# Performance work log

Hardware: AMD Instinct MI355X
Metric: run time of the kernel (lower is better)

The kernel has to match this reference:

```python
import jax, jax.numpy as jnp
import numpy as np

NH = 4        # router attention heads
M1, M2 = 16, 16  # Fourier modes kept
N_FNO_LAYERS = 4
TOP_K = 2
TEMP = 1.0


def _ln(x, g, b):
    m = x.mean(-1, keepdims=True)
    v = ((x - m) ** 2).mean(-1, keepdims=True)
    return (x - m) / jnp.sqrt(v + 1e-5) * g + b


def _mha(s, wqkv, bqkv, wo, bo):
    B, S, D = s.shape
    dh = D // NH
    qkv = s @ wqkv + bqkv
    q, k, v = jnp.split(qkv, 3, axis=-1)
    rs = lambda t: t.reshape(B, S, NH, dh).transpose(0, 2, 1, 3)
    q, k, v = rs(q), rs(k), rs(v)
    a = jax.nn.softmax(jnp.einsum('bhqd,bhkd->bhqk', q, k) / np.sqrt(dh), axis=-1)
    o = jnp.einsum('bhqk,bhkd->bhqd', a, v).transpose(0, 2, 1, 3).reshape(B, S, D)
    return o @ wo + bo


def _spectral_conv(h, w1, w2):
    # h: (B, Ci, H, W); w1/w2: (Ci, Co, M1, M2, 2) real/imag pairs
    B, Ci, H, W = h.shape
    Co = w1.shape[1]
    ft = jnp.fft.rfft2(h, axes=(-2, -1))  # (B, Ci, H, W//2+1) complex
    w1c = w1[..., 0] + 1j * w1[..., 1]
    w2c = w2[..., 0] + 1j * w2[..., 1]
    lo = jnp.einsum('bixy,ioxy->boxy', ft[:, :, :M1, :M2], w1c)
    hi = jnp.einsum('bixy,ioxy->boxy', ft[:, :, -M1:, :M2], w2c)
    oft = jnp.zeros((B, Co, H, W // 2 + 1), dtype=ft.dtype)
    oft = oft.at[:, :, :M1, :M2].set(lo).at[:, :, -M1:, :M2].set(hi)
    return jnp.fft.irfft2(oft, s=(H, W), axes=(-2, -1))


def _fno(x, lw, lb, sw1, sw2, kw, kb, p1w, p1b, p2w, p2b):
    h = jnp.einsum('bchw,co->bohw', x, lw) + lb[None, :, None, None]
    for l in range(N_FNO_LAYERS):
        s = _spectral_conv(h, sw1[l], sw2[l])
        sk = jnp.einsum('bchw,co->bohw', h, kw[l]) + kb[l][None, :, None, None]
        h = s + sk
        if l < N_FNO_LAYERS - 1:
            h = jax.nn.gelu(h)
    h = jax.nn.gelu(jnp.einsum('bchw,co->bohw', h, p1w) + p1b[None, :, None, None])
    return jnp.einsum('bchw,co->bohw', h, p2w) + p2b[None, :, None, None]


def _router(x, enc_in_w, enc_in_b, attn_wqkv, attn_bqkv, attn_wo, attn_bo,
            ln1_g, ln1_b, ffn_w1, ffn_b1, ffn_w2, ffn_b2, ln2_g, ln2_b, fc_w, fc_b):
    ic = x[:, :, 0, :]                       # (B, C, W) initial condition
    s = ic.transpose(0, 2, 1) @ enc_in_w + enc_in_b  # (B, W, hd)
    for l in range(attn_wqkv.shape[0]):
        s = _ln(s + _mha(s, attn_wqkv[l], attn_bqkv[l], attn_wo[l], attn_bo[l]), ln1_g[l], ln1_b[l])
        f = jax.nn.relu(s @ ffn_w1[l] + ffn_b1[l]) @ ffn_w2[l] + ffn_b2[l]
        s = _ln(s + f, ln2_g[l], ln2_b[l])
    feat = s.max(axis=1)                     # global max-pool over sequence
    logits = feat @ fc_w + fc_b              # (B, E)
    vals, idx = jax.lax.top_k(logits, TOP_K)
    w = jax.nn.softmax(vals / TEMP, axis=-1)
    B = logits.shape[0]
    rw = jnp.zeros_like(logits).at[jnp.arange(B)[:, None], idx].set(w)
    return rw


def setup_inputs() -> dict:
    key = jax.random.key(0)
    ks = iter(jax.random.split(key, 40))
    B, C, H, W = 32, 1, 64, 64
    E, HC, HD, RL, FF, OC = 8, 64, 64, 2, 256, 1
    rn = lambda shp, sc: jax.random.normal(next(ks), shp, dtype=jnp.float32) * sc
    inp = {
        'x': rn((B, C, H, W), 1.0),
        'enc_in_w': rn((C, HD), 0.5), 'enc_in_b': jnp.zeros((HD,), jnp.float32),
        'attn_wqkv': rn((RL, HD, 3 * HD), 0.08), 'attn_bqkv': jnp.zeros((RL, 3 * HD), jnp.float32),
        'attn_wo': rn((RL, HD, HD), 0.08), 'attn_bo': jnp.zeros((RL, HD), jnp.float32),
        'ln1_g': jnp.ones((RL, HD), jnp.float32), 'ln1_b': jnp.zeros((RL, HD), jnp.float32),
        'ffn_w1': rn((RL, HD, FF), 0.08), 'ffn_b1': jnp.zeros((RL, FF), jnp.float32),
        'ffn_w2': rn((RL, FF, HD), 0.05), 'ffn_b2': jnp.zeros((RL, HD), jnp.float32),
        'ln2_g': jnp.ones((RL, HD), jnp.float32), 'ln2_b': jnp.zeros((RL, HD), jnp.float32),
        'fc_w': rn((HD, E), 0.1), 'fc_b': jnp.zeros((E,), jnp.float32),
        'lift_w': rn((E, C, HC), 0.3), 'lift_b': jnp.zeros((E, HC), jnp.float32),
        'spec_w1': rn((E, N_FNO_LAYERS, HC, HC, M1, M2, 2), 1.0 / HC),
        'spec_w2': rn((E, N_FNO_LAYERS, HC, HC, M1, M2, 2), 1.0 / HC),
        'skip_w': rn((E, N_FNO_LAYERS, HC, HC), 0.08), 'skip_b': jnp.zeros((E, N_FNO_LAYERS, HC), jnp.float32),
        'proj1_w': rn((E, HC, HC), 0.08), 'proj1_b': jnp.zeros((E, HC), jnp.float32),
        'proj2_w': rn((E, HC, OC), 0.08), 'proj2_b': jnp.zeros((E, OC), jnp.float32),
    }
    return inp


def reference(x, enc_in_w, enc_in_b, attn_wqkv, attn_bqkv, attn_wo, attn_bo,
              ln1_g, ln1_b, ffn_w1, ffn_b1, ffn_w2, ffn_b2, ln2_g, ln2_b, fc_w, fc_b,
              lift_w, lift_b, spec_w1, spec_w2, skip_w, skip_b,
              proj1_w, proj1_b, proj2_w, proj2_b):
    rw = _router(x, enc_in_w, enc_in_b, attn_wqkv, attn_bqkv, attn_wo, attn_bo,
                 ln1_g, ln1_b, ffn_w1, ffn_b1, ffn_w2, ffn_b2, ln2_g, ln2_b, fc_w, fc_b)
    E = rw.shape[1]
    out = jnp.zeros((x.shape[0], proj2_w.shape[2], x.shape[2], x.shape[3]), x.dtype)
    for e in range(E):
        # weight is 0 for non-selected experts, so dense weighted sum == masked dispatch
        y = _fno(x, lift_w[e], lift_b[e], spec_w1[e], spec_w2[e],
                 skip_w[e], skip_b[e], proj1_w[e], proj1_b[e], proj2_w[e], proj2_b[e])
        out = out + rw[:, e, None, None, None] * y
    return out
```

## Files before the change

kernel.cpp:

```cpp
#include <hip/hip_runtime.h>
#include <math.h>

#define TWOPI_F 6.283185307179586f
#define LD4(p) (*(const float4*)(p))

__device__ __forceinline__ float gelu_f(float v) {
    float u = 0.7978845608028654f * (v + 0.044715f * v * v * v);
    return 0.5f * v * (1.f + tanhf(u));
}

__global__ void init_tables_kernel(float* __restrict__ Wy, float* __restrict__ TWX,
                                   float* __restrict__ WY2) {
    int t = threadIdx.x;
    for (int i = t; i < 1024; i += 256) {
        int y = i >> 4, k = i & 15;
        int m = (k * y) & 63;
        float a = -TWOPI_F * (float)m / 64.f;
        Wy[y * 32 + 2 * k]     = cosf(a);
        Wy[y * 32 + 2 * k + 1] = sinf(a);
    }
    if (t < 64) {
        float a = -TWOPI_F * (float)t / 64.f;
        TWX[2 * t]           = cosf(a);
        TWX[2 * t + 1]       = sinf(a);
        TWX[128 + 2 * t]     = cosf(a);
        TWX[128 + 2 * t + 1] = -sinf(a);
    }
    for (int i = t; i < 1024; i += 256) {
        int y = i >> 4, k = i & 15;
        int m = (k * y) & 63;
        float a = TWOPI_F * (float)m / 64.f;
        float sc = (k == 0 ? 1.f : 2.f) / 4096.f;
        WY2[y * 32 + 2 * k]     = sc * cosf(a);
        WY2[y * 32 + 2 * k + 1] = sc * sinf(a);
    }
}

__global__ __launch_bounds__(512) void router_kernel(
    const float* __restrict__ x, const float* __restrict__ enc_w, const float* __restrict__ enc_b,
    const float* __restrict__ wqkv, const float* __restrict__ bqkv,
    const float* __restrict__ wo, const float* __restrict__ bo,
    const float* __restrict__ ln1g, const float* __restrict__ ln1b,
    const float* __restrict__ w1, const float* __restrict__ b1,
    const float* __restrict__ w2, const float* __restrict__ b2,
    const float* __restrict__ ln2g, const float* __restrict__ ln2b,
    const float* __restrict__ fcw, const float* __restrict__ fcb,
    float* __restrict__ rw)
{
    __shared__ float s[64][65];
    __shared__ float qk[64][193];
    __shared__ float scH[4][64][65];
    __shared__ float o64[64][65];
    __shared__ float feat[64];
    __shared__ float logits[8];
    int b = blockIdx.x, t = threadIdx.x;

    for (int i = t; i < 4096; i += 512) {
        int w_ = i >> 6, d = i & 63;
        s[w_][d] = x[b * 4096 + w_] * enc_w[d] + enc_b[d];
    }
    __syncthreads();

    for (int l = 0; l < 2; ++l) {
        {
            const float* Wq = wqkv + l * 64 * 192;
            const float* Bq = bqkv + l * 192;
            int c4 = t % 48, rg = t / 48;
            if (rg < 8) {
                const float* wcol = Wq + 4 * c4;
                float4 bq = LD4(Bq + 4 * c4);
                float4 acc[8];
#pragma unroll
                for (int i = 0; i < 8; ++i) acc[i] = bq;
                int r0 = rg * 8;
#pragma unroll 8
                for (int k = 0; k < 64; ++k) {
                    float4 wv = LD4(wcol + k * 192);
#pragma unroll
                    for (int i = 0; i < 8; ++i) {
                        float sv = s[r0 + i][k];
                        acc[i].x += sv * wv.x; acc[i].y += sv * wv.y;
                        acc[i].z += sv * wv.z; acc[i].w += sv * wv.w;
                    }
                }
#pragma unroll
                for (int i = 0; i < 8; ++i) {
                    qk[r0 + i][4 * c4]     = acc[i].x;
                    qk[r0 + i][4 * c4 + 1] = acc[i].y;
                    qk[r0 + i][4 * c4 + 2] = acc[i].z;
                    qk[r0 + i][4 * c4 + 3] = acc[i].w;
                }
            }
        }
        __syncthreads();
        for (int i = t; i < 16384; i += 512) {
            int h = i >> 12, q = (i >> 6) & 63, kj = i & 63;
            float acc = 0.f;
#pragma unroll
            for (int d = 0; d < 16; ++d)
                acc += qk[q][h * 16 + d] * qk[kj][64 + h * 16 + d];
            scH[h][q][kj] = acc * 0.25f;
        }
        __syncthreads();
        if (t < 256) {
            int h = t >> 6, q = t & 63;
            float* row = scH[h][q];
            float m = -1e30f;
            for (int j = 0; j < 64; ++j) m = fmaxf(m, row[j]);
            float sum = 0.f;
            for (int j = 0; j < 64; ++j) { float e2 = expf(row[j] - m); row[j] = e2; sum += e2; }
            float inv = 1.f / sum;
            for (int j = 0; j < 64; ++j) row[j] *= inv;
        }
        __syncthreads();
        for (int i = t; i < 4096; i += 512) {
            int q = i >> 6, d = i & 63, h = d >> 4;
            float acc = 0.f;
#pragma unroll 8
            for (int j = 0; j < 64; ++j) acc += scH[h][q][j] * qk[j][128 + d];
            o64[q][d] = acc;
        }
        __syncthreads();
        {
            const float* Wo = wo + l * 4096;
            const float* Bo = bo + l * 64;
            int c4 = t & 15, rg = t >> 4;
            const float* wcol = Wo + 4 * c4;
            float4 acc0 = LD4(Bo + 4 * c4), acc1 = acc0;
            int r0 = rg * 2;
#pragma unroll 8
            for (int k = 0; k < 64; ++k) {
                float4 wv = LD4(wcol + k * 64);
                float h0 = o64[r0][k], h1 = o64[r0 + 1][k];
                acc0.x += h0 * wv.x; acc0.y += h0 * wv.y;
                acc0.z += h0 * wv.z; acc0.w += h0 * wv.w;
                acc1.x += h1 * wv.x; acc1.y += h1 * wv.y;
                acc1.z += h1 * wv.z; acc1.w += h1 * wv.w;
            }
            scH[0][r0][4 * c4]     = s[r0][4 * c4]     + acc0.x;
            scH[0][r0][4 * c4 + 1] = s[r0][4 * c4 + 1] + acc0.y;
            scH[0][r0][4 * c4 + 2] = s[r0][4 * c4 + 2] + acc0.z;
            scH[0][r0][4 * c4 + 3] = s[r0][4 * c4 + 3] + acc0.w;
            scH[0][r0 + 1][4 * c4]     = s[r0 + 1][4 * c4]     + acc1.x;
            scH[0][r0 + 1][4 * c4 + 1] = s[r0 + 1][4 * c4 + 1] + acc1.y;
            scH[0][r0 + 1][4 * c4 + 2] = s[r0 + 1][4 * c4 + 2] + acc1.z;
            scH[0][r0 + 1][4 * c4 + 3] = s[r0 + 1][4 * c4 + 3] + acc1.w;
        }
        __syncthreads();
        if (t < 64) {
            float m = 0.f;
            for (int j = 0; j < 64; ++j) m += scH[0][t][j];
            m *= (1.f / 64.f);
            float v = 0.f;
            for (int j = 0; j < 64; ++j) { float d = scH[0][t][j] - m; v += d * d; }
            v *= (1.f / 64.f);
            float inv = rsqrtf(v + 1e-5f);
            for (int j = 0; j < 64; ++j)
                s[t][j] = (scH[0][t][j] - m) * inv * ln1g[l * 64 + j] + ln1b[l * 64 + j];
        }
        __syncthreads();
        {
            const float* W1 = w1 + l * 64 * 256;
            const float* B1 = b1 + l * 256;
            int c4 = t & 63, rg = t >> 6;
            const float* wcol = W1 + 4 * c4;
            float4 b1v = LD4(B1 + 4 * c4);
            float4 acc[8];
#pragma unroll
            for (int i = 0; i < 8; ++i) acc[i] = b1v;
            int r0 = rg * 8;
#pragma unroll 4
            for (int k = 0; k < 64; ++k) {
                float4 wv = LD4(wcol + k * 256);
#pragma unroll
                for (int i = 0; i < 8; ++i) {
                    float sv = s[r0 + i][k];
                    acc[i].x += sv * wv.x; acc[i].y += sv * wv.y;
                    acc[i].z += sv * wv.z; acc[i].w += sv * wv.w;
                }
            }
#pragma unroll
            for (int i = 0; i < 8; ++i) {
                float a0 = fmaxf(acc[i].x, 0.f), a1 = fmaxf(acc[i].y, 0.f);
                float a2 = fmaxf(acc[i].z, 0.f), a3 = fmaxf(acc[i].w, 0.f);
                if (c4 < 48) {
                    qk[r0 + i][4 * c4] = a0; qk[r0 + i][4 * c4 + 1] = a1;
                    qk[r0 + i][4 * c4 + 2] = a2; qk[r0 + i][4 * c4 + 3] = a3;
                } else {
                    int c = 4 * c4 - 192;
                    o64[r0 + i][c] = a0; o64[r0 + i][c + 1] = a1;
                    o64[r0 + i][c + 2] = a2; o64[r0 + i][c + 3] = a3;
                }
            }
        }
        __syncthreads();
        {
            const float* W2 = w2 + l * 256 * 64;
            const float* B2 = b2 + l * 64;
            int c4 = t & 15, rg = t >> 4;
            const float* wcol = W2 + 4 * c4;
            float4 acc0 = LD4(B2 + 4 * c4), acc1 = acc0;
            int r0 = rg * 2;
#pragma unroll 8
            for (int k = 0; k < 192; ++k) {
                float4 wv = LD4(wcol + k * 64);
                float h0 = qk[r0][k], h1 = qk[r0 + 1][k];
                acc0.x += h0 * wv.x; acc0.y += h0 * wv.y;
                acc0.z += h0 * wv.z; acc0.w += h0 * wv.w;
                acc1.x += h1 * wv.x; acc1.y += h1 * wv.y;
                acc1.z += h1 * wv.z; acc1.w += h1 * wv.w;
            }
#pragma unroll 8
            for (int k = 192; k < 256; ++k) {
                float4 wv = LD4(wcol + k * 64);
                float h0 = o64[r0][k - 192], h1 = o64[r0 + 1][k - 192];
                acc0.x += h0 * wv.x; acc0.y += h0 * wv.y;
                acc0.z += h0 * wv.z; acc0.w += h0 * wv.w;
                acc1.x += h1 * wv.x; acc1.y += h1 * wv.y;
                acc1.z += h1 * wv.z; acc1.w += h1 * wv.w;
            }
            scH[0][r0][4 * c4]     = s[r0][4 * c4]     + acc0.x;
            scH[0][r0][4 * c4 + 1] = s[r0][4 * c4 + 1] + acc0.y;
            scH[0][r0][4 * c4 + 2] = s[r0][4 * c4 + 2] + acc0.z;
            scH[0][r0][4 * c4 + 3] = s[r0][4 * c4 + 3] + acc0.w;
            scH[0][r0 + 1][4 * c4]     = s[r0 + 1][4 * c4]     + acc1.x;
            scH[0][r0 + 1][4 * c4 + 1] = s[r0 + 1][4 * c4 + 1] + acc1.y;
            scH[0][r0 + 1][4 * c4 + 2] = s[r0 + 1][4 * c4 + 2] + acc1.z;
            scH[0][r0 + 1][4 * c4 + 3] = s[r0 + 1][4 * c4 + 3] + acc1.w;
        }
        __syncthreads();
        if (t < 64) {
            float m = 0.f;
            for (int j = 0; j < 64; ++j) m += scH[0][t][j];
            m *= (1.f / 64.f);
            float v = 0.f;
            for (int j = 0; j < 64; ++j) { float d = scH[0][t][j] - m; v += d * d; }
            v *= (1.f / 64.f);
            float inv = rsqrtf(v + 1e-5f);
            for (int j = 0; j < 64; ++j)
                s[t][j] = (scH[0][t][j] - m) * inv * ln2g[l * 64 + j] + ln2b[l * 64 + j];
        }
        __syncthreads();
    }
    if (t < 64) {
        float m = -1e30f;
        for (int r = 0; r < 64; ++r) m = fmaxf(m, s[r][t]);
        feat[t] = m;
    }
    __syncthreads();
    if (t < 8) {
        float acc = fcb[t];
        for (int k = 0; k < 64; ++k) acc += feat[k] * fcw[k * 8 + t];
        logits[t] = acc;
    }
    __syncthreads();
    if (t == 0) {
        int i0 = 0;
        for (int j = 1; j < 8; ++j) if (logits[j] > logits[i0]) i0 = j;
        int i1 = -1;
        for (int j = 0; j < 8; ++j) {
            if (j == i0) continue;
            if (i1 < 0 || logits[j] > logits[i1]) i1 = j;
        }
        float e1 = expf(logits[i1] - logits[i0]);
        float w0 = 1.f / (1.f + e1);
        float w1v = e1 / (1.f + e1);
        for (int j = 0; j < 8; ++j) rw[b * 8 + j] = 0.f;
        rw[b * 8 + i0] = w0;
        rw[b * 8 + i1] = w1v;
    }
}

__global__ void build_pairs_kernel(const float* __restrict__ rw, int* __restrict__ pair_b,
                                   int* __restrict__ pair_e, float* __restrict__ pair_w,
                                   int* __restrict__ estart, int* __restrict__ chunk_e,
                                   int* __restrict__ chunk_p0, int* __restrict__ chunk_np) {
    __shared__ float r[256];
    __shared__ int cnt[8], off[9];
    int t = threadIdx.x;
    for (int i = t; i < 256; i += 64) r[i] = rw[i];
    if (t < 64) { pair_b[t] = 0; pair_e[t] = 0; pair_w[t] = 0.f; }
    __syncthreads();
    if (t < 8) {
        int c = 0;
        for (int b = 0; b < 32; ++b) if (r[b * 8 + t] != 0.f) ++c;
        cnt[t] = c;
    }
    __syncthreads();
    if (t == 0) {
        int a = 0;
        for (int e = 0; e < 8; ++e) { off[e] = a; a += cnt[e]; }
        off[8] = a;
        for (int e = 0; e <= 8; ++e) estart[e] = off[e];
        int nc = 0;
        for (int e = 0; e < 8; ++e) {
            for (int s = off[e]; s < off[e + 1]; s += 8) {
                int np = off[e + 1] - s; if (np > 8) np = 8;
                chunk_e[nc] = e; chunk_p0[nc] = s; chunk_np[nc] = np; ++nc;
            }
        }
        for (int c = nc; c < 16; ++c) { chunk_e[c] = 0; chunk_p0[c] = 0; chunk_np[c] = 0; }
    }
    __syncthreads();
    if (t < 8) {
        int n = off[t];
        for (int b = 0; b < 32; ++b) {
            float w = r[b * 8 + t];
            if (w != 0.f) { pair_b[n] = b; pair_e[n] = t; pair_w[n] = w; ++n; }
        }
    }
}

__global__ __launch_bounds__(256) void fwdft_conv_kernel(
    const float* __restrict__ h, const float* __restrict__ Wy,
    const float* __restrict__ TWX, float* __restrict__ F,
    float* __restrict__ dst, const float* __restrict__ skw,
    const float* __restrict__ skb, const int* __restrict__ pair_e, int l)
{
    __shared__ __align__(16) char smem[35328];
    int t = threadIdx.x;
    if (blockIdx.x < 4096) {
        float (*ht)[68] = (float(*)[68])(smem);
        float (*gt)[36] = (float(*)[36])(smem + 17408);
        float* wy   = (float*)(smem + 26624);
        float* tw64 = (float*)(smem + 34816);
        int bid = blockIdx.x;
        const float* src = h + (size_t)bid * 4096;
        for (int i = t; i < 1024; i += 256) {
            float4 v = LD4(src + i * 4);
            int xx = (i * 4) >> 6, y = (i * 4) & 63;
            *(float4*)(&ht[xx][y]) = v;
        }
        for (int i = t; i < 512; i += 256) *(float4*)(&wy[i * 4]) = LD4(Wy + i * 4);
        if (t < 32) *(float4*)(&tw64[t * 4]) = LD4(TWX + t * 4);
        __syncthreads();
        {
            int xx = t >> 2, kq = t & 3;
            float gr0 = 0.f, gi0 = 0.f, gr1 = 0.f, gi1 = 0.f;
            float gr2 = 0.f, gi2 = 0.f, gr3 = 0.f, gi3 = 0.f;
#pragma unroll 4
            for (int y = 0; y < 64; ++y) {
                float hv = ht[xx][y];
                float4 w0 = *(const float4*)(&wy[y * 32 + kq * 8]);
                float4 w1 = *(const float4*)(&wy[y * 32 + kq * 8 + 4]);
                gr0 += hv * w0.x; gi0 += hv * w0.y;
                gr1 += hv * w0.z; gi1 += hv * w0.w;
                gr2 += hv * w1.x; gi2 += hv * w1.y;
                gr3 += hv * w1.z; gi3 += hv * w1.w;
            }
            *(float4*)(&gt[xx][kq * 8])     = make_float4(gr0, gi0, gr1, gi1);
            *(float4*)(&gt[xx][kq * 8 + 4]) = make_float4(gr2, gi2, gr3, gi3);
        }
        __syncthreads();
        {
            int kxm = t & 31, kyq = t >> 5;
            int kx = kxm < 16 ? kxm : kxm + 32;
            float ar0 = 0.f, ai0 = 0.f, ar1 = 0.f, ai1 = 0.f;
            int idx = 0;
#pragma unroll 4
            for (int xx = 0; xx < 64; ++xx) {
                float c_ = tw64[2 * idx], s_ = tw64[2 * idx + 1];
                float4 g = *(const float4*)(&gt[xx][kyq * 4]);
                ar0 += g.x * c_ - g.y * s_;  ai0 += g.x * s_ + g.y * c_;
                ar1 += g.z * c_ - g.w * s_;  ai1 += g.z * s_ + g.w * c_;
                idx = (idx + kx) & 63;
            }
            float* fb = F + (size_t)bid * 1024 + kxm * 32 + kyq * 4;
            *(float4*)(fb) = make_float4(ar0, ai0, ar1, ai1);
        }
    } else {
        float (*ws)[68] = (float(*)[68])(smem);
        float* bs = (float*)(smem + 17408);
        int idx = blockIdx.x - 4096;
        int p = idx >> 4, tile = idx & 15;
        int e = pair_e[p];
        int widx = e * 4 + l;
        const float* W = skw + (size_t)widx * 4096;
        for (int i = t; i < 1024; i += 256) {
            float4 v = LD4(W + i * 4);
            int ci = (i * 4) >> 6, co = (i * 4) & 63;
            *(float4*)(&ws[ci][co]) = v;
        }
        if (t < 64) bs[t] = skb[widx * 64 + t];
        __syncthreads();

        int xy4 = t & 63, cog = t >> 6;
        const float* sb = h + (size_t)p * 262144 + tile * 256 + xy4 * 4;
        float4 acc[16];
#pragma unroll
        for (int j = 0; j < 16; ++j) {
            float bv = bs[cog * 16 + j];
            acc[j] = make_float4(bv, bv, bv, bv);
        }
        for (int ci = 0; ci < 64; ++ci) {
            float4 sv = LD4(sb + (size_t)ci * 4096);
            float4 w0 = *(const float4*)(&ws[ci][cog * 16]);
            float4 w1 = *(const float4*)(&ws[ci][cog * 16 + 4]);
            float4 w2 = *(const float4*)(&ws[ci][cog * 16 + 8]);
            float4 w3 = *(const float4*)(&ws[ci][cog * 16 + 12]);
            float wr[16] = {w0.x, w0.y, w0.z, w0.w, w1.x, w1.y, w1.z, w1.w,
                            w2.x, w2.y, w2.z, w2.w, w3.x, w3.y, w3.z, w3.w};
#pragma unroll
            for (int j = 0; j < 16; ++j) {
                float w = wr[j];
                acc[j].x += sv.x * w; acc[j].y += sv.y * w;
                acc[j].z += sv.z * w; acc[j].w += sv.w * w;
            }
        }
        float* d = dst + (size_t)p * 262144 + (size_t)(cog * 16) * 4096 + tile * 256 + xy4 * 4;
#pragma unroll
        for (int j = 0; j < 16; ++j)
            *(float4*)(d + (size_t)j * 4096) = acc[j];
    }
}

__global__ __launch_bounds__(256) void fwdftx_convx_kernel(
    const float* __restrict__ x, const float* __restrict__ lw,
    const float* __restrict__ lb, const int* __restrict__ pair_b,
    const int* __restrict__ pair_e, const float* __restrict__ Wy,
    const float* __restrict__ TWX, float* __restrict__ F,
    float* __restrict__ dst, const float* __restrict__ skw,
    const float* __restrict__ skb)
{
    __shared__ __align__(16) char smem[35328];
    int t = threadIdx.x;
    if (blockIdx.x < 4096) {
        float (*ht)[68] = (float(*)[68])(smem);
        float (*gt)[36] = (float(*)[36])(smem + 17408);
        float* wy   = (float*)(smem + 26624);
        float* tw64 = (float*)(smem + 34816);
        int bid = blockIdx.x;
        int p = bid >> 6, ci = bid & 63;
        int e = pair_e[p], b = pair_b[p];
        float lwv = lw[e * 64 + ci];
        float lbv = lb[e * 64 + ci];
        const float* src = x + (size_t)b * 4096;
        for (int i = t; i < 1024; i += 256) {
            float4 v = LD4(src + i * 4);
            v.x = v.x * lwv + lbv; v.y = v.y * lwv + lbv;
            v.z = v.z * lwv + lbv; v.w = v.w * lwv + lbv;
            int xx = (i * 4) >> 6, y = (i * 4) & 63;
            *(float4*)(&ht[xx][y]) = v;
        }
        for (int i = t; i < 512; i += 256) *(float4*)(&wy[i * 4]) = LD4(Wy + i * 4);
        if (t < 32) *(float4*)(&tw64[t * 4]) = LD4(TWX + t * 4);
        __syncthreads();
        {
            int xx = t >> 2, kq = t & 3;
            float gr0 = 0.f, gi0 = 0.f, gr1 = 0.f, gi1 = 0.f;
            float gr2 = 0.f, gi2 = 0.f, gr3 = 0.f, gi3 = 0.f;
#pragma unroll 4
            for (int y = 0; y < 64; ++y) {
                float hv = ht[xx][y];
                float4 w0 = *(const float4*)(&wy[y * 32 + kq * 8]);
                float4 w1 = *(const float4*)(&wy[y * 32 + kq * 8 + 4]);
                gr0 += hv * w0.x; gi0 += hv * w0.y;
                gr1 += hv * w0.z; gi1 += hv * w0.w;
                gr2 += hv * w1.x; gi2 += hv * w1.y;
                gr3 += hv * w1.z; gi3 += hv * w1.w;
            }
            *(float4*)(&gt[xx][kq * 8])     = make_float4(gr0, gi0, gr1, gi1);
            *(float4*)(&gt[xx][kq * 8 + 4]) = make_float4(gr2, gi2, gr3, gi3);
        }
        __syncthreads();
        {
            int kxm = t & 31, kyq = t >> 5;
            int kx = kxm < 16 ? kxm : kxm + 32;
            float ar0 = 0.f, ai0 = 0.f, ar1 = 0.f, ai1 = 0.f;
            int idx = 0;
#pragma unroll 4
            for (int xx = 0; xx < 64; ++xx) {
                float c_ = tw64[2 * idx], s_ = tw64[2 * idx + 1];
                float4 g = *(const float4*)(&gt[xx][kyq * 4]);
                ar0 += g.x * c_ - g.y * s_;  ai0 += g.x * s_ + g.y * c_;
                ar1 += g.z * c_ - g.w * s_;  ai1 += g.z * s_ + g.w * c_;
                idx = (idx + kx) & 63;
            }
            float* fb = F + (size_t)bid * 1024 + kxm * 32 + kyq * 4;
            *(float4*)(fb) = make_float4(ar0, ai0, ar1, ai1);
        }
    } else {
        float (*ws)[68] = (float(*)[68])(smem);
        float* bs  = (float*)(smem + 17408);
        float* lws = (float*)(smem + 17664);
        float* lbs = (float*)(smem + 17920);
        int idx = blockIdx.x - 4096;
        int p = idx >> 4, tile = idx & 15;
        int e = pair_e[p], b = pair_b[p];
        int widx = e * 4;
        const float* W = skw + (size_t)widx * 4096;
        for (int i = t; i < 1024; i += 256) {
            float4 v = LD4(W + i * 4);
            int ci = (i * 4) >> 6, co = (i * 4) & 63;
            *(float4*)(&ws[ci][co]) = v;
        }
        if (t < 64) {
            bs[t]  = skb[widx * 64 + t];
            lws[t] = lw[e * 64 + t];
            lbs[t] = lb[e * 64 + t];
        }
        __syncthreads();

        int xy4 = t & 63, cog = t >> 6;
        float4 xv = LD4(x + (size_t)b * 4096 + tile * 256 + xy4 * 4);
        float4 acc[16];
#pragma unroll
        for (int j = 0; j < 16; ++j) {
            float bv = bs[cog * 16 + j];
            acc[j] = make_float4(bv, bv, bv, bv);
        }
        for (int ci = 0; ci < 64; ++ci) {
            float lwv = lws[ci], lbv = lbs[ci];
            float4 sv = make_float4(xv.x * lwv + lbv, xv.y * lwv + lbv,
                                    xv.z * lwv + lbv, xv.w * lwv + lbv);
            float4 w0 = *(const float4*)(&ws[ci][cog * 16]);
            float4 w1 = *(const float4*)(&ws[ci][cog * 16 + 4]);
            float4 w2 = *(const float4*)(&ws[ci][cog * 16 + 8]);
            float4 w3 = *(const float4*)(&ws[ci][cog * 16 + 12]);
            float wr[16] = {w0.x, w0.y, w0.z, w0.w, w1.x, w1.y, w1.z, w1.w,
                            w2.x, w2.y, w2.z, w2.w, w3.x, w3.y, w3.z, w3.w};
#pragma unroll
            for (int j = 0; j < 16; ++j) {
                float w = wr[j];
                acc[j].x += sv.x * w; acc[j].y += sv.y * w;
                acc[j].z += sv.z * w; acc[j].w += sv.w * w;
            }
        }
        float* d = dst + (size_t)p * 262144 + (size_t)(cog * 16) * 4096 + tile * 256 + xy4 * 4;
#pragma unroll
        for (int j = 0; j < 16; ++j)
            *(float4*)(d + (size_t)j * 4096) = acc[j];
    }
}

__global__ __launch_bounds__(256) void spectral_kernel(
    const float* __restrict__ F, float* __restrict__ FoA, float* __restrict__ FoB,
    const float* __restrict__ w1, const float* __restrict__ w2,
    const int* __restrict__ chunk_e, const int* __restrict__ chunk_p0,
    const int* __restrict__ chunk_np, int l)
{
    int c = blockIdx.x;
    int np = chunk_np[c];
    if (np == 0) return;
    int e = chunk_e[c], p0 = chunk_p0[c];
    int z = blockIdx.z;
    int wsel = z & 1, cih = (z >> 1) & 1, mq = z >> 2;
    int t = threadIdx.x;
    int co = blockIdx.y * 4 + (t >> 6);
    int lane = t & 63;
    int moff = mq * 256 + lane * 4;

    const float* wbase = (wsel == 0 ? w1 : w2) + (size_t)(e * 4 + l) * 2097152;
    const float* Wc  = wbase + (size_t)(cih * 32) * 32768 + (size_t)co * 512 + moff;
    const float* Fc0 = F + (size_t)p0 * 65536 + (size_t)(cih * 32) * 1024 + wsel * 512 + moff;
    float* Fob = (cih ? FoB : FoA) + (size_t)p0 * 65536 + (size_t)co * 1024 + wsel * 512 + moff;

    float4 acc[8];
#pragma unroll
    for (int p = 0; p < 8; ++p) acc[p] = make_float4(0.f, 0.f, 0.f, 0.f);
    const float* Wp = Wc;
    const float* Fp = Fc0;
    for (int ci = 0; ci < 32; ++ci) {
        float4 wv = LD4(Wp);
#pragma unroll
        for (int p = 0; p < 8; ++p) {
            float4 fv = LD4(Fp + (size_t)p * 65536);
            acc[p].x += fv.x * wv.x - fv.y * wv.y;
            acc[p].y += fv.x * wv.y + fv.y * wv.x;
            acc[p].z += fv.z * wv.z - fv.w * wv.w;
            acc[p].w += fv.z * wv.w + fv.w * wv.z;
        }
        Wp += 32768;
        Fp += 1024;
    }
#pragma unroll
    for (int p = 0; p < 8; ++p) {
        if (p < np)
            *(float4*)(Fob + (size_t)p * 65536) = acc[p];
    }
}

__global__ __launch_bounds__(256) void projfused_kernel(
    const float* __restrict__ src, const float* __restrict__ p1w,
    const float* __restrict__ p1b, const float* __restrict__ p2w,
    const float* __restrict__ p2b, const int* __restrict__ pair_b,
    const int* __restrict__ pair_e, const float* __restrict__ pw,
    float* __restrict__ out)
{
    __shared__ float ws[64][68];
    __shared__ float bs[64];
    __shared__ float w2s[64];
    __shared__ float4 red[4][64];
    int p = blockIdx.x, tile = blockIdx.y, t = threadIdx.x;
    int e = pair_e[p];
    const float* W = p1w + (size_t)e * 4096;
    for (int i = t; i < 1024; i += 256) {
        float4 v = LD4(W + i * 4);
        int ci = (i * 4) >> 6, co = (i * 4) & 63;
        *(float4*)(&ws[ci][co]) = v;
    }
    if (t < 64) { bs[t] = p1b[e * 64 + t]; w2s[t] = p2w[e * 64 + t]; }
    __syncthreads();

    int xy4 = t & 63, cog = t >> 6;
    const float* sb = src + (size_t)p * 262144 + tile * 256 + xy4 * 4;
    float4 acc[16];
#pragma unroll
    for (int j = 0; j < 16; ++j) {
        float bv = bs[cog * 16 + j];
        acc[j] = make_float4(bv, bv, bv, bv);
    }
    for (int ci = 0; ci < 64; ++ci) {
        float4 sv = LD4(sb + (size_t)ci * 4096);
        float4 w0 = *(const float4*)(&ws[ci][cog * 16]);
        float4 w1 = *(const float4*)(&ws[ci][cog * 16 + 4]);
        float4 w2 = *(const float4*)(&ws[ci][cog * 16 + 8]);
        float4 w3 = *(const float4*)(&ws[ci][cog * 16 + 12]);
        float wr[16] = {w0.x, w0.y, w0.z, w0.w, w1.x, w1.y, w1.z, w1.w,
                        w2.x, w2.y, w2.z, w2.w, w3.x, w3.y, w3.z, w3.w};
#pragma unroll
        for (int j = 0; j < 16; ++j) {
            float w = wr[j];
            acc[j].x += sv.x * w; acc[j].y += sv.y * w;
            acc[j].z += sv.z * w; acc[j].w += sv.w * w;
        }
    }
    float4 part = make_float4(0.f, 0.f, 0.f, 0.f);
#pragma unroll
    for (int j = 0; j < 16; ++j) {
        float w = w2s[cog * 16 + j];
        part.x += gelu_f(acc[j].x) * w;
        part.y += gelu_f(acc[j].y) * w;
        part.z += gelu_f(acc[j].z) * w;
        part.w += gelu_f(acc[j].w) * w;
    }
    red[cog][xy4] = part;
    __syncthreads();
    if (t < 64) {
        float4 s0 = red[0][t], s1 = red[1][t], s2 = red[2][t], s3 = red[3][t];
        float wgt = pw[p];
        float b2 = p2b[e];
        int b = pair_b[p];
        float* ob = out + (size_t)b * 4096 + tile * 256 + t * 4;
        atomicAdd(ob,     wgt * (s0.x + s1.x + s2.x + s3.x + b2));
        atomicAdd(ob + 1, wgt * (s0.y + s1.y + s2.y + s3.y + b2));
        atomicAdd(ob + 2, wgt * (s0.z + s1.z + s2.z + s3.z + b2));
        atomicAdd(ob + 3, wgt * (s0.w + s1.w + s2.w + s3.w + b2));
    }
}

__global__ __launch_bounds__(256) void inv_kernel(
    const float* __restrict__ FoA, const float* __restrict__ FoB,
    const float* __restrict__ WY2, const float* __restrict__ TWX,
    float* __restrict__ dst_h, int do_gelu)
{
    __shared__ float wy2[2048];
    __shared__ float twl[128];
    __shared__ float fo_s[1024];
    __shared__ float tT[64][36];
    __shared__ float ot[64][66];
    int t = threadIdx.x;
    for (int i = t; i < 512; i += 256) *(float4*)(&wy2[i * 4]) = LD4(WY2 + i * 4);
    if (t < 32) *(float4*)(&twl[t * 4]) = LD4(TWX + 128 + t * 4);
    int wid = blockIdx.x;
    int p = wid >> 6, co = wid & 63;
    const float* fA = FoA + (size_t)p * 65536 + (size_t)co * 1024;
    const float* fB = FoB + (size_t)p * 65536 + (size_t)co * 1024;
    {
        float4 a = LD4(fA + t * 4);
        float4 b = LD4(fB + t * 4);
        *(float4*)(&fo_s[t * 4]) = make_float4(a.x + b.x, a.y + b.y, a.z + b.z, a.w + b.w);
    }
    __syncthreads();
    {
        int xx = t & 63, kq = t >> 6;
        float Tr0 = 0.f, Ti0 = 0.f, Tr1 = 0.f, Ti1 = 0.f;
        float Tr2 = 0.f, Ti2 = 0.f, Tr3 = 0.f, Ti3 = 0.f;
#pragma unroll 4
        for (int kxm = 0; kxm < 32; ++kxm) {
            int kx = kxm < 16 ? kxm : kxm + 32;
            int idx = (kx * xx) & 63;
            float c_ = twl[2 * idx], s_ = twl[2 * idx + 1];
            float4 f0 = *(const float4*)(&fo_s[kxm * 32 + kq * 8]);
            float4 f1 = *(const float4*)(&fo_s[kxm * 32 + kq * 8 + 4]);
            Tr0 += f0.x * c_ - f0.y * s_;  Ti0 += f0.x * s_ + f0.y * c_;
            Tr1 += f0.z * c_ - f0.w * s_;  Ti1 += f0.z * s_ + f0.w * c_;
            Tr2 += f1.x * c_ - f1.y * s_;  Ti2 += f1.x * s_ + f1.y * c_;
            Tr3 += f1.z * c_ - f1.w * s_;  Ti3 += f1.z * s_ + f1.w * c_;
        }
        *(float4*)(&tT[xx][kq * 8])     = make_float4(Tr0, Ti0, Tr1, Ti1);
        *(float4*)(&tT[xx][kq * 8 + 4]) = make_float4(Tr2, Ti2, Tr3, Ti3);
    }
    __syncthreads();
    {
        int xx = t & 63, yq = t >> 6;
        float Trr[16], Tii[16];
#pragma unroll
        for (int q = 0; q < 8; ++q) {
            float4 v = *(const float4*)(&tT[xx][q * 4]);
            Trr[q * 2] = v.x; Tii[q * 2] = v.y;
            Trr[q * 2 + 1] = v.z; Tii[q * 2 + 1] = v.w;
        }
        for (int j = 0; j < 16; ++j) {
            int y = yq * 16 + j;
            const float* wr = &wy2[y * 32];
            float acc = 0.f;
#pragma unroll
            for (int k = 0; k < 16; ++k)
                acc += Trr[k] * wr[2 * k] - Tii[k] * wr[2 * k + 1];
            ot[xx][y] = acc;
        }
    }
    __syncthreads();
    {
        float* base = dst_h + (size_t)p * 262144 + (size_t)co * 4096;
        for (int r = 0; r < 16; ++r) {
            int gidx = r * 256 + t;
            int xx = gidx >> 6, y = gidx & 63;
            float v = base[gidx] + ot[xx][y];
            if (do_gelu) v = gelu_f(v);
            base[gidx] = v;
        }
    }
}

extern "C" void kernel_launch(void* const* d_in, const int* in_sizes, int n_in,
                              void* d_out, int out_size, void* d_ws, size_t ws_size,
                              hipStream_t stream) {
    const float* x    = (const float*)d_in[0];
    const float* encw = (const float*)d_in[1];
    const float* encb = (const float*)d_in[2];
    const float* wqkv = (const float*)d_in[3];
    const float* bqkv = (const float*)d_in[4];
    const float* wo   = (const float*)d_in[5];
    const float* bo   = (const float*)d_in[6];
    const float* ln1g = (const float*)d_in[7];
    const float* ln1b = (const float*)d_in[8];
    const float* fw1  = (const float*)d_in[9];
    const float* fb1  = (const float*)d_in[10];
    const float* fw2  = (const float*)d_in[11];
    const float* fb2  = (const float*)d_in[12];
    const float* ln2g = (const float*)d_in[13];
    const float* ln2b = (const float*)d_in[14];
    const float* fcw  = (const float*)d_in[15];
    const float* fcb  = (const float*)d_in[16];
    const float* lw   = (const float*)d_in[17];
    const float* lb   = (const float*)d_in[18];
    const float* sw1  = (const float*)d_in[19];
    const float* sw2  = (const float*)d_in[20];
    const float* skw  = (const float*)d_in[21];
    const float* skb  = (const float*)d_in[22];
    const float* p1w  = (const float*)d_in[23];
    const float* p1b  = (const float*)d_in[24];
    const float* p2w  = (const float*)d_in[25];
    const float* p2b  = (const float*)d_in[26];
    float* out = (float*)d_out;

    float* wsf    = (float*)d_ws;
    float* rw     = wsf;
    float* pair_w = wsf + 256;
    int*   ipart  = (int*)(wsf + 320);
    int* pair_b   = ipart;
    int* pair_e   = ipart + 64;
    int* estart   = ipart + 128;
    int* chunk_e  = ipart + 137;
    int* chunk_p0 = ipart + 153;
    int* chunk_np = ipart + 169;
    float* Wy  = wsf + 512;
    float* TWX = wsf + 2560;
    float* WY2 = wsf + 6656;
    float* hA  = wsf + 16384;
    float* hB  = hA + (size_t)64 * 262144;
    float* F   = hB + (size_t)64 * 262144;
    float* FoA = F + (size_t)64 * 65536;
    float* FoB = FoA + (size_t)64 * 65536;
    size_t need = (16384 + 2ull * 64 * 262144 + 64ull * 65536 + 64ull * 131072) * 4;
    if (ws_size < need) return;

    hipMemsetAsync(d_out, 0, (size_t)out_size * sizeof(float), stream);
    init_tables_kernel<<<1, 256, 0, stream>>>(Wy, TWX, WY2);
    router_kernel<<<32, 512, 0, stream>>>(x, encw, encb, wqkv, bqkv, wo, bo, ln1g, ln1b,
                                          fw1, fb1, fw2, fb2, ln2g, ln2b, fcw, fcb, rw);
    build_pairs_kernel<<<1, 64, 0, stream>>>(rw, pair_b, pair_e, pair_w, estart,
                                             chunk_e, chunk_p0, chunk_np);
    for (int l = 0; l < 4; ++l) {
        float* cur = (l & 1) ? hB : hA;
        float* nxt = (l & 1) ? hA : hB;
        if (l == 0) {
            fwdftx_convx_kernel<<<5120, 256, 0, stream>>>(x, lw, lb, pair_b, pair_e,
                                                          Wy, TWX, F, nxt, skw, skb);
        } else {
            fwdft_conv_kernel<<<5120, 256, 0, stream>>>(cur, Wy, TWX, F, nxt,
                                                        skw, skb, pair_e, l);
        }
        spectral_kernel<<<dim3(16, 16, 8), 256, 0, stream>>>(F, FoA, FoB, sw1, sw2,
                                                             chunk_e, chunk_p0, chunk_np, l);
        inv_kernel<<<4096, 256, 0, stream>>>(FoA, FoB, WY2, TWX, nxt, (l < 3) ? 1 : 0);
    }
    projfused_kernel<<<dim3(64, 16), 256, 0, stream>>>(hA, p1w, p1b, p2w, p2b,
                                                       pair_b, pair_e, pair_w, out);
}
```

Before: 1.248 ms.

## Fuse forward DFT into inverse kernel and skip conv into spectral kernel

The inverse DFT kernel now also computes the forward DFT of the freshly produced (GELU'd) activation directly from shared memory. This removes the separate forward-DFT pass that re-read the full activation tensor from global memory each layer. The pointwise skip convolution moves into the spectral-mixing launch as extra blocks, which cuts one launch per layer and lets the two independent computations share the GPU. In exchange, the inverse kernel uses more shared memory, which may lower occupancy.

```diff
diff --git a/kernel.cpp b/kernel.cpp
--- a/kernel.cpp
+++ b/kernel.cpp
@@ -308,109 +308,6 @@
             float w = r[b * 8 + t];
             if (w != 0.f) { pair_b[n] = b; pair_e[n] = t; pair_w[n] = w; ++n; }
         }
-    }
-}
-
-__global__ __launch_bounds__(256) void fwdft_conv_kernel(
-    const float* __restrict__ h, const float* __restrict__ Wy,
-    const float* __restrict__ TWX, float* __restrict__ F,
-    float* __restrict__ dst, const float* __restrict__ skw,
-    const float* __restrict__ skb, const int* __restrict__ pair_e, int l)
-{
-    __shared__ __align__(16) char smem[35328];
-    int t = threadIdx.x;
-    if (blockIdx.x < 4096) {
-        float (*ht)[68] = (float(*)[68])(smem);
-        float (*gt)[36] = (float(*)[36])(smem + 17408);
-        float* wy   = (float*)(smem + 26624);
-        float* tw64 = (float*)(smem + 34816);
-        int bid = blockIdx.x;
-        const float* src = h + (size_t)bid * 4096;
-        for (int i = t; i < 1024; i += 256) {
-            float4 v = LD4(src + i * 4);
-            int xx = (i * 4) >> 6, y = (i * 4) & 63;
-            *(float4*)(&ht[xx][y]) = v;
-        }
-        for (int i = t; i < 512; i += 256) *(float4*)(&wy[i * 4]) = LD4(Wy + i * 4);
-        if (t < 32) *(float4*)(&tw64[t * 4]) = LD4(TWX + t * 4);
-        __syncthreads();
-        {
-            int xx = t >> 2, kq = t & 3;
-            float gr0 = 0.f, gi0 = 0.f, gr1 = 0.f, gi1 = 0.f;
-            float gr2 = 0.f, gi2 = 0.f, gr3 = 0.f, gi3 = 0.f;
-#pragma unroll 4
-            for (int y = 0; y < 64; ++y) {
-                float hv = ht[xx][y];
-                float4 w0 = *(const float4*)(&wy[y * 32 + kq * 8]);
-                float4 w1 = *(const float4*)(&wy[y * 32 + kq * 8 + 4]);
-                gr0 += hv * w0.x; gi0 += hv * w0.y;
-                gr1 += hv * w0.z; gi1 += hv * w0.w;
-                gr2 += hv * w1.x; gi2 += hv * w1.y;
-                gr3 += hv * w1.z; gi3 += hv * w1.w;
-            }
-            *(float4*)(&gt[xx][kq * 8])     = make_float4(gr0, gi0, gr1, gi1);
-            *(float4*)(&gt[xx][kq * 8 + 4]) = make_float4(gr2, gi2, gr3, gi3);
-        }
-        __syncthreads();
-        {
-            int kxm = t & 31, kyq = t >> 5;
-            int kx = kxm < 16 ? kxm : kxm + 32;
-            float ar0 = 0.f, ai0 = 0.f, ar1 = 0.f, ai1 = 0.f;
-            int idx = 0;
-#pragma unroll 4
-            for (int xx = 0; xx < 64; ++xx) {
-                float c_ = tw64[2 * idx], s_ = tw64[2 * idx + 1];
-                float4 g = *(const float4*)(&gt[xx][kyq * 4]);
-                ar0 += g.x * c_ - g.y * s_;  ai0 += g.x * s_ + g.y * c_;
-                ar1 += g.z * c_ - g.w * s_;  ai1 += g.z * s_ + g.w * c_;
-                idx = (idx + kx) & 63;
-            }
-            float* fb = F + (size_t)bid * 1024 + kxm * 32 + kyq * 4;
-            *(float4*)(fb) = make_float4(ar0, ai0, ar1, ai1);
-        }
-    } else {
-        float (*ws)[68] = (float(*)[68])(smem);
-        float* bs = (float*)(smem + 17408);
-        int idx = blockIdx.x - 4096;
-        int p = idx >> 4, tile = idx & 15;
-        int e = pair_e[p];
-        int widx = e * 4 + l;
-        const float* W = skw + (size_t)widx * 4096;
-        for (int i = t; i < 1024; i += 256) {
-            float4 v = LD4(W + i * 4);
-            int ci = (i * 4) >> 6, co = (i * 4) & 63;
-            *(float4*)(&ws[ci][co]) = v;
-        }
-        if (t < 64) bs[t] = skb[widx * 64 + t];
-        __syncthreads();
-
-        int xy4 = t & 63, cog = t >> 6;
-        const float* sb = h + (size_t)p * 262144 + tile * 256 + xy4 * 4;
-        float4 acc[16];
-#pragma unroll
-        for (int j = 0; j < 16; ++j) {
-            float bv = bs[cog * 16 + j];
-            acc[j] = make_float4(bv, bv, bv, bv);
-        }
-        for (int ci = 0; ci < 64; ++ci) {
-            float4 sv = LD4(sb + (size_t)ci * 4096);
-            float4 w0 = *(const float4*)(&ws[ci][cog * 16]);
-            float4 w1 = *(const float4*)(&ws[ci][cog * 16 + 4]);
-            float4 w2 = *(const float4*)(&ws[ci][cog * 16 + 8]);
-            float4 w3 = *(const float4*)(&ws[ci][cog * 16 + 12]);
-            float wr[16] = {w0.x, w0.y, w0.z, w0.w, w1.x, w1.y, w1.z, w1.w,
-                            w2.x, w2.y, w2.z, w2.w, w3.x, w3.y, w3.z, w3.w};
-#pragma unroll
-            for (int j = 0; j < 16; ++j) {
-                float w = wr[j];
-                acc[j].x += sv.x * w; acc[j].y += sv.y * w;
-                acc[j].z += sv.z * w; acc[j].w += sv.w * w;
-            }
-        }
-        float* d = dst + (size_t)p * 262144 + (size_t)(cog * 16) * 4096 + tile * 256 + xy4 * 4;
-#pragma unroll
-        for (int j = 0; j < 16; ++j)
-            *(float4*)(d + (size_t)j * 4096) = acc[j];
     }
 }
 
@@ -580,6 +477,221 @@
     }
 }
 
+__global__ __launch_bounds__(256) void spectral_conv_kernel(
+    const float* __restrict__ F, float* __restrict__ FoA, float* __restrict__ FoB,
+    const float* __restrict__ w1, const float* __restrict__ w2,
+    const int* __restrict__ chunk_e, const int* __restrict__ chunk_p0,
+    const int* __restrict__ chunk_np,
+    const float* __restrict__ h, float* __restrict__ dst,
+    const float* __restrict__ skw, const float* __restrict__ skb,
+    const int* __restrict__ pair_e, int l)
+{
+    __shared__ __align__(16) char smem[17664];
+    int t = threadIdx.x;
+    if (blockIdx.x < 2048) {
+        int bid = blockIdx.x;
+        int c = bid & 15, coy = (bid >> 4) & 15, z = bid >> 8;
+        int np = chunk_np[c];
+        if (np == 0) return;
+        int e = chunk_e[c], p0 = chunk_p0[c];
+        int wsel = z & 1, cih = (z >> 1) & 1, mq = z >> 2;
+        int co = coy * 4 + (t >> 6);
+        int lane = t & 63;
+        int moff = mq * 256 + lane * 4;
+
+        const float* wbase = (wsel == 0 ? w1 : w2) + (size_t)(e * 4 + l) * 2097152;
+        const float* Wc  = wbase + (size_t)(cih * 32) * 32768 + (size_t)co * 512 + moff;
+        const float* Fc0 = F + (size_t)p0 * 65536 + (size_t)(cih * 32) * 1024 + wsel * 512 + moff;
+        float* Fob = (cih ? FoB : FoA) + (size_t)p0 * 65536 + (size_t)co * 1024 + wsel * 512 + moff;
+
+        float4 acc[8];
+#pragma unroll
+        for (int p = 0; p < 8; ++p) acc[p] = make_float4(0.f, 0.f, 0.f, 0.f);
+        const float* Wp = Wc;
+        const float* Fp = Fc0;
+        for (int ci = 0; ci < 32; ++ci) {
+            float4 wv = LD4(Wp);
+#pragma unroll
+            for (int p = 0; p < 8; ++p) {
+                float4 fv = LD4(Fp + (size_t)p * 65536);
+                acc[p].x += fv.x * wv.x - fv.y * wv.y;
+                acc[p].y += fv.x * wv.y + fv.y * wv.x;
+                acc[p].z += fv.z * wv.z - fv.w * wv.w;
+                acc[p].w += fv.z * wv.w + fv.w * wv.z;
+            }
+            Wp += 32768;
+            Fp += 1024;
+        }
+#pragma unroll
+        for (int p = 0; p < 8; ++p) {
+            if (p < np)
+                *(float4*)(Fob + (size_t)p * 65536) = acc[p];
+        }
+    } else {
+        float (*ws)[68] = (float(*)[68])(smem);
+        float* bs = (float*)(smem + 17408);
+        int idx = blockIdx.x - 2048;
+        int p = idx >> 4, tile = idx & 15;
+        int e = pair_e[p];
+        int widx = e * 4 + l;
+        const float* W = skw + (size_t)widx * 4096;
+        for (int i = t; i < 1024; i += 256) {
+            float4 v = LD4(W + i * 4);
+            int ci = (i * 4) >> 6, co = (i * 4) & 63;
+            *(float4*)(&ws[ci][co]) = v;
+        }
+        if (t < 64) bs[t] = skb[widx * 64 + t];
+        __syncthreads();
+
+        int xy4 = t & 63, cog = t >> 6;
+        const float* sb = h + (size_t)p * 262144 + tile * 256 + xy4 * 4;
+        float4 acc[16];
+#pragma unroll
+        for (int j = 0; j < 16; ++j) {
+            float bv = bs[cog * 16 + j];
+            acc[j] = make_float4(bv, bv, bv, bv);
+        }
+        for (int ci = 0; ci < 64; ++ci) {
+            float4 sv = LD4(sb + (size_t)ci * 4096);
+            float4 w0 = *(const float4*)(&ws[ci][cog * 16]);
+            float4 w1 = *(const float4*)(&ws[ci][cog * 16 + 4]);
+            float4 w2 = *(const float4*)(&ws[ci][cog * 16 + 8]);
+            float4 w3 = *(const float4*)(&ws[ci][cog * 16 + 12]);
+            float wr[16] = {w0.x, w0.y, w0.z, w0.w, w1.x, w1.y, w1.z, w1.w,
+                            w2.x, w2.y, w2.z, w2.w, w3.x, w3.y, w3.z, w3.w};
+#pragma unroll
+            for (int j = 0; j < 16; ++j) {
+                float w = wr[j];
+                acc[j].x += sv.x * w; acc[j].y += sv.y * w;
+                acc[j].z += sv.z * w; acc[j].w += sv.w * w;
+            }
+        }
+        float* d = dst + (size_t)p * 262144 + (size_t)(cog * 16) * 4096 + tile * 256 + xy4 * 4;
+#pragma unroll
+        for (int j = 0; j < 16; ++j)
+            *(float4*)(d + (size_t)j * 4096) = acc[j];
+    }
+}
+
+__global__ __launch_bounds__(256) void invfwd_kernel(
+    const float* __restrict__ FoA, const float* __restrict__ FoB,
+    const float* __restrict__ WY2, const float* __restrict__ TWX,
+    const float* __restrict__ Wy,
+    float* __restrict__ dst_h, float* __restrict__ F, int do_fwd)
+{
+    __shared__ float wy2[2048];
+    __shared__ float twl[128];
+    __shared__ float fo_s[1024];
+    __shared__ float tT[64][36];
+    __shared__ float ot[64][66];
+    __shared__ float wyf[2048];
+    __shared__ float twf[128];
+    int t = threadIdx.x;
+    for (int i = t; i < 512; i += 256) *(float4*)(&wy2[i * 4]) = LD4(WY2 + i * 4);
+    if (t < 32) *(float4*)(&twl[t * 4]) = LD4(TWX + 128 + t * 4);
+    if (do_fwd) {
+        for (int i = t; i < 512; i += 256) *(float4*)(&wyf[i * 4]) = LD4(Wy + i * 4);
+        if (t < 32) *(float4*)(&twf[t * 4]) = LD4(TWX + t * 4);
+    }
+    int wid = blockIdx.x;
+    int p = wid >> 6, co = wid & 63;
+    const float* fA = FoA + (size_t)p * 65536 + (size_t)co * 1024;
+    const float* fB = FoB + (size_t)p * 65536 + (size_t)co * 1024;
+    {
+        float4 a = LD4(fA + t * 4);
+        float4 b = LD4(fB + t * 4);
+        *(float4*)(&fo_s[t * 4]) = make_float4(a.x + b.x, a.y + b.y, a.z + b.z, a.w + b.w);
+    }
+    __syncthreads();
+    {
+        int xx = t & 63, kq = t >> 6;
+        float Tr0 = 0.f, Ti0 = 0.f, Tr1 = 0.f, Ti1 = 0.f;
+        float Tr2 = 0.f, Ti2 = 0.f, Tr3 = 0.f, Ti3 = 0.f;
+#pragma unroll 4
+        for (int kxm = 0; kxm < 32; ++kxm) {
+            int kx = kxm < 16 ? kxm : kxm + 32;
+            int idx = (kx * xx) & 63;
+            float c_ = twl[2 * idx], s_ = twl[2 * idx + 1];
+            float4 f0 = *(const float4*)(&fo_s[kxm * 32 + kq * 8]);
+            float4 f1 = *(const float4*)(&fo_s[kxm * 32 + kq * 8 + 4]);
+            Tr0 += f0.x * c_ - f0.y * s_;  Ti0 += f0.x * s_ + f0.y * c_;
+            Tr1 += f0.z * c_ - f0.w * s_;  Ti1 += f0.z * s_ + f0.w * c_;
+            Tr2 += f1.x * c_ - f1.y * s_;  Ti2 += f1.x * s_ + f1.y * c_;
+            Tr3 += f1.z * c_ - f1.w * s_;  Ti3 += f1.z * s_ + f1.w * c_;
+        }
+        *(float4*)(&tT[xx][kq * 8])     = make_float4(Tr0, Ti0, Tr1, Ti1);
+        *(float4*)(&tT[xx][kq * 8 + 4]) = make_float4(Tr2, Ti2, Tr3, Ti3);
+    }
+    __syncthreads();
+    {
+        int xx = t & 63, yq = t >> 6;
+        float Trr[16], Tii[16];
+#pragma unroll
+        for (int q = 0; q < 8; ++q) {
+            float4 v = *(const float4*)(&tT[xx][q * 4]);
+            Trr[q * 2] = v.x; Tii[q * 2] = v.y;
+            Trr[q * 2 + 1] = v.z; Tii[q * 2 + 1] = v.w;
+        }
+        for (int j = 0; j < 16; ++j) {
+            int y = yq * 16 + j;
+            const float* wr = &wy2[y * 32];
+            float acc = 0.f;
+#pragma unroll
+            for (int k = 0; k < 16; ++k)
+                acc += Trr[k] * wr[2 * k] - Tii[k] * wr[2 * k + 1];
+            ot[xx][y] = acc;
+        }
+    }
+    __syncthreads();
+    {
+        float* base = dst_h + (size_t)p * 262144 + (size_t)co * 4096;
+        for (int r = 0; r < 16; ++r) {
+            int gidx = r * 256 + t;
+            int xx = gidx >> 6, y = gidx & 63;
+            float v = base[gidx] + ot[xx][y];
+            if (do_fwd) v = gelu_f(v);
+            base[gidx] = v;
+            ot[xx][y] = v;
+        }
+    }
+    if (!do_fwd) return;
+    __syncthreads();
+    {
+        int xx = t >> 2, kq = t & 3;
+        float gr0 = 0.f, gi0 = 0.f, gr1 = 0.f, gi1 = 0.f;
+        float gr2 = 0.f, gi2 = 0.f, gr3 = 0.f, gi3 = 0.f;
+#pragma unroll 4
+        for (int y = 0; y < 64; ++y) {
+            float hv = ot[xx][y];
+            float4 w0 = *(const float4*)(&wyf[y * 32 + kq * 8]);
+            float4 w1 = *(const float4*)(&wyf[y * 32 + kq * 8 + 4]);
+            gr0 += hv * w0.x; gi0 += hv * w0.y;
+            gr1 += hv * w0.z; gi1 += hv * w0.w;
+            gr2 += hv * w1.x; gi2 += hv * w1.y;
+            gr3 += hv * w1.z; gi3 += hv * w1.w;
+        }
+        *(float4*)(&tT[xx][kq * 8])     = make_float4(gr0, gi0, gr1, gi1);
+        *(float4*)(&tT[xx][kq * 8 + 4]) = make_float4(gr2, gi2, gr3, gi3);
+    }
+    __syncthreads();
+    {
+        int kxm = t & 31, kyq = t >> 5;
+        int kx = kxm < 16 ? kxm : kxm + 32;
+        float ar0 = 0.f, ai0 = 0.f, ar1 = 0.f, ai1 = 0.f;
+        int idx = 0;
+#pragma unroll 4
+        for (int xx = 0; xx < 64; ++xx) {
+            float c_ = twf[2 * idx], s_ = twf[2 * idx + 1];
+            float4 g = *(const float4*)(&tT[xx][kyq * 4]);
+            ar0 += g.x * c_ - g.y * s_;  ai0 += g.x * s_ + g.y * c_;
+            ar1 += g.z * c_ - g.w * s_;  ai1 += g.z * s_ + g.w * c_;
+            idx = (idx + kx) & 63;
+        }
+        float* fb = F + (size_t)wid * 1024 + kxm * 32 + kyq * 4;
+        *(float4*)(fb) = make_float4(ar0, ai0, ar1, ai1);
+    }
+}
+
 __global__ __launch_bounds__(256) void projfused_kernel(
     const float* __restrict__ src, const float* __restrict__ p1w,
     const float* __restrict__ p1b, const float* __restrict__ p2w,
@@ -646,81 +758,6 @@
         atomicAdd(ob + 1, wgt * (s0.y + s1.y + s2.y + s3.y + b2));
         atomicAdd(ob + 2, wgt * (s0.z + s1.z + s2.z + s3.z + b2));
         atomicAdd(ob + 3, wgt * (s0.w + s1.w + s2.w + s3.w + b2));
-    }
-}
-
-__global__ __launch_bounds__(256) void inv_kernel(
-    const float* __restrict__ FoA, const float* __restrict__ FoB,
-    const float* __restrict__ WY2, const float* __restrict__ TWX,
-    float* __restrict__ dst_h, int do_gelu)
-{
-    __shared__ float wy2[2048];
-    __shared__ float twl[128];
-    __shared__ float fo_s[1024];
-    __shared__ float tT[64][36];
-    __shared__ float ot[64][66];
-    int t = threadIdx.x;
-    for (int i = t; i < 512; i += 256) *(float4*)(&wy2[i * 4]) = LD4(WY2 + i * 4);
-    if (t < 32) *(float4*)(&twl[t * 4]) = LD4(TWX + 128 + t * 4);
-    int wid = blockIdx.x;
-    int p = wid >> 6, co = wid & 63;
-    const float* fA = FoA + (size_t)p * 65536 + (size_t)co * 1024;
-    const float* fB = FoB + (size_t)p * 65536 + (size_t)co * 1024;
-    {
-        float4 a = LD4(fA + t * 4);
-        float4 b = LD4(fB + t * 4);
-        *(float4*)(&fo_s[t * 4]) = make_float4(a.x + b.x, a.y + b.y, a.z + b.z, a.w + b.w);
-    }
-    __syncthreads();
-    {
-        int xx = t & 63, kq = t >> 6;
-        float Tr0 = 0.f, Ti0 = 0.f, Tr1 = 0.f, Ti1 = 0.f;
-        float Tr2 = 0.f, Ti2 = 0.f, Tr3 = 0.f, Ti3 = 0.f;
-#pragma unroll 4
-        for (int kxm = 0; kxm < 32; ++kxm) {
-            int kx = kxm < 16 ? kxm : kxm + 32;
-            int idx = (kx * xx) & 63;
-            float c_ = twl[2 * idx], s_ = twl[2 * idx + 1];
-            float4 f0 = *(const float4*)(&fo_s[kxm * 32 + kq * 8]);
-            float4 f1 = *(const float4*)(&fo_s[kxm * 32 + kq * 8 + 4]);
-            Tr0 += f0.x * c_ - f0.y * s_;  Ti0 += f0.x * s_ + f0.y * c_;
-            Tr1 += f0.z * c_ - f0.w * s_;  Ti1 += f0.z * s_ + f0.w * c_;
-            Tr2 += f1.x * c_ - f1.y * s_;  Ti2 += f1.x * s_ + f1.y * c_;
-            Tr3 += f1.z * c_ - f1.w * s_;  Ti3 += f1.z * s_ + f1.w * c_;
-        }
-        *(float4*)(&tT[xx][kq * 8])     = make_float4(Tr0, Ti0, Tr1, Ti1);
-        *(float4*)(&tT[xx][kq * 8 + 4]) = make_float4(Tr2, Ti2, Tr3, Ti3);
-    }
-    __syncthreads();
-    {
-        int xx = t & 63, yq = t >> 6;
-        float Trr[16], Tii[16];
-#pragma unroll
-        for (int q = 0; q < 8; ++q) {
-            float4 v = *(const float4*)(&tT[xx][q * 4]);
-            Trr[q * 2] = v.x; Tii[q * 2] = v.y;
-            Trr[q * 2 + 1] = v.z; Tii[q * 2 + 1] = v.w;
-        }
-        for (int j = 0; j < 16; ++j) {
-            int y = yq * 16 + j;
-            const float* wr = &wy2[y * 32];
-            float acc = 0.f;
-#pragma unroll
-            for (int k = 0; k < 16; ++k)
-                acc += Trr[k] * wr[2 * k] - Tii[k] * wr[2 * k + 1];
-            ot[xx][y] = acc;
-        }
-    }
-    __syncthreads();
-    {
-        float* base = dst_h + (size_t)p * 262144 + (size_t)co * 4096;
-        for (int r = 0; r < 16; ++r) {
-            int gidx = r * 256 + t;
-            int xx = gidx >> 6, y = gidx & 63;
-            float v = base[gidx] + ot[xx][y];
-            if (do_gelu) v = gelu_f(v);
-            base[gidx] = v;
-        }
     }
 }
 
@@ -783,19 +820,19 @@
                                           fw1, fb1, fw2, fb2, ln2g, ln2b, fcw, fcb, rw);
     build_pairs_kernel<<<1, 64, 0, stream>>>(rw, pair_b, pair_e, pair_w, estart,
                                              chunk_e, chunk_p0, chunk_np);
-    for (int l = 0; l < 4; ++l) {
+    fwdftx_convx_kernel<<<5120, 256, 0, stream>>>(x, lw, lb, pair_b, pair_e,
+                                                  Wy, TWX, F, hB, skw, skb);
+    spectral_kernel<<<dim3(16, 16, 8), 256, 0, stream>>>(F, FoA, FoB, sw1, sw2,
+                                                         chunk_e, chunk_p0, chunk_np, 0);
+    invfwd_kernel<<<4096, 256, 0, stream>>>(FoA, FoB, WY2, TWX, Wy, hB, F, 1);
+    for (int l = 1; l < 4; ++l) {
         float* cur = (l & 1) ? hB : hA;
         float* nxt = (l & 1) ? hA : hB;
-        if (l == 0) {
-            fwdftx_convx_kernel<<<5120, 256, 0, stream>>>(x, lw, lb, pair_b, pair_e,
-                                                          Wy, TWX, F, nxt, skw, skb);
-        } else {
-            fwdft_conv_kernel<<<5120, 256, 0, stream>>>(cur, Wy, TWX, F, nxt,
-                                                        skw, skb, pair_e, l);
-        }
-        spectral_kernel<<<dim3(16, 16, 8), 256, 0, stream>>>(F, FoA, FoB, sw1, sw2,
-                                                             chunk_e, chunk_p0, chunk_np, l);
-        inv_kernel<<<4096, 256, 0, stream>>>(FoA, FoB, WY2, TWX, nxt, (l < 3) ? 1 : 0);
+        spectral_conv_kernel<<<3072, 256, 0, stream>>>(F, FoA, FoB, sw1, sw2,
+                                                       chunk_e, chunk_p0, chunk_np,
+                                                       cur, nxt, skw, skb, pair_e, l);
+        invfwd_kernel<<<4096, 256, 0, stream>>>(FoA, FoB, WY2, TWX, Wy, nxt, F,
+                                                (l < 3) ? 1 : 0);
     }
     projfused_kernel<<<dim3(64, 16), 256, 0, stream>>>(hA, p1w, p1b, p2w, p2b,
                                                        pair_b, pair_e, pair_w, out);
```

Measured after the change: 1.271 ms. No clear change (+1.9%).
